# Kernel optimization log

Measured on AMD Instinct MI355X. Metric: run time of the kernel, lower is better.

The kernel has to match this reference:

```python
import jax, jax.numpy as jnp
import numpy as np

NEG_SLOPE = 0.2


def setup_inputs() -> dict:
    key = jax.random.key(0)
    kx, ka, kW, kav = jax.random.split(key, 4)
    B, V, H, D = 8, 2048, 256, 128
    x = jax.random.normal(kx, (B, V, H), dtype=jnp.float32)
    adjacency_matrix = jax.random.randint(ka, (V, V), 0, 2, dtype=jnp.int32)
    W = jax.random.normal(kW, (D, H), dtype=jnp.float32) * 0.05  # Linear(H->D), weight [out,in]
    a = jax.random.normal(kav, (1, 2 * D), dtype=jnp.float32) * 0.05  # Linear(2D->1)
    return {"x": x, "adjacency_matrix": adjacency_matrix, "W": W, "a": a}


def reference(x, adjacency_matrix, W, a):
    B, V, H = x.shape
    D = W.shape[0]
    # p = W(x): [B,V,D]
    p = jnp.einsum('bvh,dh->bvd', x, W)
    # a(cat(p_i, p_j)) == a_left.p_i + a_right.p_j ; leaky_relu applied to the sum (same math,
    # avoids materializing the O(B*V^2*2D) repeat/concat tensor)
    a_left, a_right = a[0, :D], a[0, D:]
    e_i = p @ a_left    # [B,V]
    e_j = p @ a_right   # [B,V]
    scores = jax.nn.leaky_relu(e_i[:, :, None] + e_j[:, None, :], negative_slope=NEG_SLOPE)  # [B,V,V]
    weights = jax.nn.softmax(scores, axis=-1)
    adj = adjacency_matrix.astype(weights.dtype)[None]  # [1,V,V]
    weights_masked = weights * adj
    # renormalize masked weights to the (unmasked) row mass
    weights_masked = weights_masked * (
        jnp.sum(weights, axis=-1, keepdims=True) / jnp.sum(weights_masked, axis=-1, keepdims=True)
    )
    # weighted sum over neighbors j: sum_j w[b,i,j] * p[b,j,:]
    attentioned = jnp.einsum('bij,bjd->bid', weights_masked, p)
    return jax.nn.relu(attentioned)
```

## Files before the change

kernel.cpp:

```cpp
#include <hip/hip_runtime.h>
#include <hip/hip_bf16.h>

#define BATCH 8
#define V 2048
#define H 256
#define D 128

typedef __attribute__((ext_vector_type(8))) _Float16 f16x8;
typedef __attribute__((ext_vector_type(4))) float f32x4;
typedef unsigned int uint32;

static __device__ __forceinline__ uint32 pk2(float lo, float hi) {
  __fp16 __attribute__((ext_vector_type(2))) h = __builtin_amdgcn_cvt_pkrtz(lo, hi);
  uint32 u;
  __builtin_memcpy(&u, &h, 4);
  return u;
}

__global__ __launch_bounds__(256) void k_pack(const int* __restrict__ adj,
                                              const float* __restrict__ W,
                                              const float* __restrict__ a,
                                              unsigned int* __restrict__ pkT,
                                              float* __restrict__ vL,
                                              float* __restrict__ vR,
                                              _Float16* __restrict__ Wh) {
  const int blk = blockIdx.x;
  if (blk < V) {
    const int w = threadIdx.x >> 6, lane = threadIdx.x & 63;
    const int* row = adj + (size_t)blk * V;
#pragma unroll
    for (int it = 0; it < 8; ++it) {
      const int j = it * 256 + w * 64 + lane;
      unsigned long long m = __ballot(row[j] != 0);
      if (lane < 2) {
        const int jw = it * 8 + w * 2 + lane;
        pkT[(size_t)jw * V + blk] = (unsigned int)(m >> (lane * 32));
      }
    }
  } else if (blk == V) {
    const int h = threadIdx.x;
    float sL = 0.f, sR = 0.f;
    for (int d = 0; d < D; ++d) {
      const float wv = W[(size_t)d * H + h];
      sL += wv * a[d];
      sR += wv * a[D + d];
    }
    vL[h] = sL;
    vR[h] = sR;
  } else {
    const int t = threadIdx.x;
    for (int i = 0; i < D; ++i)
      Wh[(size_t)i * H + t] = (_Float16)W[(size_t)i * H + t];
  }
}

__global__ __launch_bounds__(256, 2) void k_proj(const float* __restrict__ x,
                                                 const _Float16* __restrict__ Wh,
                                                 const float* __restrict__ vL,
                                                 const float* __restrict__ vR,
                                                 _Float16* __restrict__ pTf,
                                                 float* __restrict__ ei,
                                                 _Float16* __restrict__ Fh,
                                                 _Float16* __restrict__ Ph) {
  __shared__ char xls[32 * 512];
  __shared__ _Float16 st[128][52];
  const int t = threadIdx.x, lane = t & 63, wave = t >> 6;
  const int b = blockIdx.x >> 6;
  const int jt0 = blockIdx.x & 63;
  const int j0 = jt0 * 32;
  const int kq = lane >> 4, l15 = lane & 15;

  {
    const float4 vl4 = *(const float4*)(vL + lane * 4);
    const float4 vr4 = *(const float4*)(vR + lane * 4);
#pragma unroll
    for (int rr = 0; rr < 8; ++rr) {
      const int row = wave * 8 + rr;
      const float4 xv = *(const float4*)(x + ((size_t)(b * V + j0 + row)) * H + lane * 4);
      uint32 u0 = pk2(xv.x, xv.y), u1 = pk2(xv.z, xv.w);
      const int off = row * 512 + ((lane * 8) ^ ((row & 7) << 4));
      *(uint32*)(xls + off) = u0;
      *(uint32*)(xls + off + 4) = u1;
      float eL = xv.x * vl4.x + xv.y * vl4.y + xv.z * vl4.z + xv.w * vl4.w;
      float eR = xv.x * vr4.x + xv.y * vr4.y + xv.z * vr4.z + xv.w * vr4.w;
#pragma unroll
      for (int off_ = 1; off_ < 64; off_ <<= 1) {
        eL += __shfl_xor(eL, off_, 64);
        eR += __shfl_xor(eR, off_, 64);
      }
      if (lane == 0) {
        const size_t r_ = (size_t)b * V + j0 + row;
        ei[r_] = eL;
        Fh[r_] = (_Float16)__expf(eR);
        Ph[r_] = (_Float16)__expf(0.2f * eR);
      }
    }
  }
  __syncthreads();

  f32x4 acc[2][2];
#pragma unroll
  for (int i_ = 0; i_ < 2; ++i_)
#pragma unroll
    for (int j_ = 0; j_ < 2; ++j_) acc[i_][j_] = (f32x4){0.f, 0.f, 0.f, 0.f};

  const char* wbase = (const char*)Wh + ((size_t)(wave * 32 + l15) * H + kq * 8) * 2;
#pragma unroll
  for (int ks = 0; ks < 8; ++ks) {
    f16x8 aw[2], bx[2];
#pragma unroll
    for (int t_ = 0; t_ < 2; ++t_)
      aw[t_] = *(const f16x8*)(wbase + (t_ * 16 * H + ks * 32) * 2);
#pragma unroll
    for (int jt = 0; jt < 2; ++jt) {
      const int row = jt * 16 + l15;
      bx[jt] = *(const f16x8*)(xls + row * 512 + ((ks * 64 + kq * 16) ^ ((l15 & 7) << 4)));
    }
#pragma unroll
    for (int t_ = 0; t_ < 2; ++t_)
#pragma unroll
      for (int jt = 0; jt < 2; ++jt)
        acc[t_][jt] = __builtin_amdgcn_mfma_f32_16x16x32_f16(aw[t_], bx[jt], acc[t_][jt], 0, 0, 0);
  }

#pragma unroll
  for (int t_ = 0; t_ < 2; ++t_)
#pragma unroll
    for (int jt = 0; jt < 2; ++jt)
#pragma unroll
      for (int r = 0; r < 4; ++r)
        st[(wave * 2 + t_) * 16 + kq * 4 + r][jt * 16 + l15] = (_Float16)acc[t_][jt][r];
  __syncthreads();

  const int c = jt0 >> 1;
  const int ksh = jt0 & 1;
  const int g = t >> 6;
#pragma unroll
  for (int ff = 0; ff < 2; ++ff) {
    const int dt = ff * 4 + g;
    const int dR = dt * 16 + l15;
    const int jc = kq * 8;
    union { unsigned long long ll[2]; f16x8 v; } vv_;
    vv_.ll[0] = *(const unsigned long long*)&st[dR][jc];
    vv_.ll[1] = *(const unsigned long long*)&st[dR][jc + 4];
    *(f16x8*)((char*)pTf +
              (((((size_t)b * 32 + c) * 8 + dt) * 2 + ksh) * 64 + lane) * 16) = vv_.v;
  }
}


typedef union { uint4 v; uint32 u[4]; } U4;
typedef union { uint32 u[4]; f16x8 v; } AFu;
struct PFS {
  U4 FH0, FH1, PH0, PH1;
  uint32 w[2][2];
  AFu AF[2][2];
};

#define PKMUL(d, a, b) asm("v_pk_mul_f16 %0, %1, %2" : "=v"(d) : "v"(a), "v"(b));
#define PKMAX(d, a, b) asm("v_pk_max_f16 %0, %1, %2" : "=v"(d) : "v"(a), "v"(b));

#define WGEN(S)                                                        \
  _Pragma("unroll") for (int ig_ = 0; ig_ < 2; ++ig_) {                \
    const uint32 E2_ = Ei2g[ig_], EP2_ = Eip2g[ig_];                   \
    _Pragma("unroll") for (int ks_ = 0; ks_ < 2; ++ks_) {              \
      const uint32 sh_ = (S).w[ig_][ks_] >> kq8;                       \
      _Pragma("unroll") for (int p_ = 0; p_ < 4; ++p_) {               \
        uint32 t0_, t1_;                                               \
        PKMUL(t0_, E2_, (ks_ ? (S).FH1 : (S).FH0).u[p_])               \
        PKMUL(t1_, EP2_, (ks_ ? (S).PH1 : (S).PH0).u[p_])              \
        PKMAX(t0_, t0_, t1_)                                           \
        const uint32 m_ = ((sh_ << (14 - 2 * p_)) & 0x4000u) |         \
                          ((sh_ << (29 - 2 * p_)) & 0x40000000u);      \
        PKMUL((S).AF[ig_][ks_].u[p_], t0_, m_)                         \
      }                                                                \
    }                                                                  \
  }

#define PFETCH(S, C)                                       \
  {                                                        \
    const char* f_ = fbase + (C) * 128 + kq16;             \
    const char* p_ = pbase + (C) * 128 + kq16;             \
    (S).FH0.v = *(const uint4*)(f_);                       \
    (S).FH1.v = *(const uint4*)(f_ + 64);                  \
    (S).PH0.v = *(const uint4*)(p_);                       \
    (S).PH1.v = *(const uint4*)(p_ + 64);                  \
    (S).w[0][0] = adjpT[(size_t)((C) * 2) * V + iR0];      \
    (S).w[0][1] = adjpT[(size_t)((C) * 2 + 1) * V + iR0];  \
    (S).w[1][0] = adjpT[(size_t)((C) * 2) * V + iR1];      \
    (S).w[1][1] = adjpT[(size_t)((C) * 2 + 1) * V + iR1];  \
  }

#define LOADB(BR, C)                                      \
  {                                                       \
    const char* g_ = gbase + (size_t)(C) * 16384;         \
    _Pragma("unroll") for (int q_ = 0; q_ < 4; ++q_)      \
      BR[q_] = *(const f16x8*)(g_ + q_ * 1024);           \
  }

#define DOMFMA(S, BX)                                                          \
  _Pragma("unroll") for (int ig_ = 0; ig_ < 2; ++ig_)                          \
    _Pragma("unroll") for (int nt_ = 0; nt_ < 2; ++nt_)                        \
      _Pragma("unroll") for (int ks_ = 0; ks_ < 2; ++ks_)                      \
        acc[ig_][nt_][ks_] = __builtin_amdgcn_mfma_f32_16x16x32_f16(           \
            (S).AF[ig_][ks_].v, BX[nt_ * 2 + ks_], acc[ig_][nt_][ks_], 0, 0, 0); \
  _Pragma("unroll") for (int ig_ = 0; ig_ < 2; ++ig_)                          \
    _Pragma("unroll") for (int ks_ = 0; ks_ < 2; ++ks_)                        \
      accS[ig_][ks_] = __builtin_amdgcn_mfma_f32_16x16x32_f16(                 \
          (S).AF[ig_][ks_].v, onesv, accS[ig_][ks_], 0, 0, 0);

#define BODYF(C, SX, BX, SY)   \
  {                            \
    DOMFMA(SX, BX)             \
    WGEN(SY)                   \
    LOADB(BX, (C) + 2)         \
    PFETCH(SX, (C) + 2)        \
  }

__global__ __launch_bounds__(256, 2) void k_attn(
    const _Float16* __restrict__ pTf,
    const float* __restrict__ ei,
    const _Float16* __restrict__ Fht,
    const _Float16* __restrict__ Pht,
    const unsigned int* __restrict__ adjpT,
    float* __restrict__ out) {
  const int t = threadIdx.x, lane = t & 63, wave = t >> 6;
  const int ih = wave >> 1;
  const int dq = wave & 1;
  const int pay = (blockIdx.x & 7) * 64 + (blockIdx.x >> 3);
  const int bdh = pay >> 4;
  const int itl = pay & 15;
  const int b = bdh >> 2, dh = (bdh >> 1) & 1;
  const int it = ((bdh & 1) << 4) | itl;
  const int i0b = it * 64;
  const int kq = lane >> 4;
  const int kq8 = kq * 8;
  const int kq16 = kq * 16;
  const int l15 = lane & 15;
  const int ibase = i0b + ih * 32;
  const int iR0 = ibase + l15;
  const int iR1 = iR0 + 16;

  const float eiv0 = ei[(size_t)b * V + iR0];
  const float eiv1 = ei[(size_t)b * V + iR1];
  uint32 Ei2g[2], Eip2g[2];
  {
    const float e0 = 0.5f * __expf(eiv0), e1 = 0.5f * __expf(eiv1);
    const float p0 = 0.5f * __expf(0.2f * eiv0), p1 = 0.5f * __expf(0.2f * eiv1);
    Ei2g[0] = pk2(e0, e0); Ei2g[1] = pk2(e1, e1);
    Eip2g[0] = pk2(p0, p0); Eip2g[1] = pk2(p1, p1);
  }
  const char* fbase = (const char*)(Fht + (size_t)b * V);
  const char* pbase = (const char*)(Pht + (size_t)b * V);
  const size_t fb0 = ((size_t)b * 32) * 16384 + (size_t)dh * 8192;
  const char* gbase = (const char*)pTf + fb0 + dq * 4096 + lane * 16;

  union { uint32 u[4]; f16x8 v; } ones_;
  ones_.u[0] = ones_.u[1] = ones_.u[2] = ones_.u[3] = 0x3C003C00u;
  const f16x8 onesv = ones_.v;

  f32x4 acc[2][2][2];
#pragma unroll
  for (int a_ = 0; a_ < 2; ++a_)
#pragma unroll
    for (int b_ = 0; b_ < 2; ++b_)
#pragma unroll
      for (int c_ = 0; c_ < 2; ++c_) acc[a_][b_][c_] = (f32x4){0.f, 0.f, 0.f, 0.f};
  f32x4 accS[2][2];
#pragma unroll
  for (int a_ = 0; a_ < 2; ++a_)
#pragma unroll
    for (int c_ = 0; c_ < 2; ++c_) accS[a_][c_] = (f32x4){0.f, 0.f, 0.f, 0.f};

  f16x8 bA[4], bB[4];
  PFS sA, sB;

  LOADB(bA, 0)
  LOADB(bB, 1)
  PFETCH(sA, 0)
  PFETCH(sB, 1)
  WGEN(sA)

  for (int c2 = 0; c2 < 15; ++c2) {
    const int c = c2 * 2;
    BODYF(c, sA, bA, sB)
    BODYF(c + 1, sB, bB, sA)
  }
  {
    DOMFMA(sA, bA)
    WGEN(sB)
  }
  { DOMFMA(sB, bB) }

  float* ob = out + ((size_t)b * V + ibase) * D + dh * 64 + dq * 32 + l15;
#pragma unroll
  for (int ig = 0; ig < 2; ++ig) {
#pragma unroll
    for (int r = 0; r < 4; ++r) {
      const float inv_ = 1.0f / (accS[ig][0][r] + accS[ig][1][r]);
#pragma unroll
      for (int nt = 0; nt < 2; ++nt) {
        const float v = (acc[ig][nt][0][r] + acc[ig][nt][1][r]) * inv_;
        ob[(size_t)(ig * 16 + kq * 4 + r) * D + nt * 16] = fmaxf(v, 0.f);
      }
    }
  }
}

extern "C" void kernel_launch(void* const* d_in, const int* in_sizes, int n_in,
                              void* d_out, int out_size, void* d_ws, size_t ws_size,
                              hipStream_t stream) {
  const float* x = (const float*)d_in[0];
  const int* adj = (const int*)d_in[1];
  const float* W = (const float*)d_in[2];
  const float* a = (const float*)d_in[3];
  float* out = (float*)d_out;

  char* ws = (char*)d_ws;
  _Float16* pTf = (_Float16*)ws;
  float* ei = (float*)(ws + (4u << 20));
  _Float16* Fh = (_Float16*)(ws + (4u << 20) + 65536);
  _Float16* Ph = (_Float16*)(ws + (4u << 20) + 98304);
  unsigned int* adjpT = (unsigned int*)(ws + (4u << 20) + 131072);
  float* vL = (float*)(ws + (4u << 20) + 655360);
  float* vR = (float*)(ws + (4u << 20) + 656384);
  _Float16* Wh = (_Float16*)(ws + (4u << 20) + 657408);

  k_pack<<<dim3(V + 2), dim3(256), 0, stream>>>(adj, W, a, adjpT, vL, vR, Wh);
  k_proj<<<dim3(BATCH * (V / 32)), dim3(256), 0, stream>>>(x, Wh, vL, vR, pTf, ei, Fh, Ph);
  k_attn<<<dim3(BATCH * 2 * (V / 64)), dim3(256), 0, stream>>>(pTf, ei, Fh, Ph, adjpT, out);
}
```

Measured before the change: 54.46 us.

## Split attention over neighbor halves with partial sums and a reduce kernel

The attention kernel now splits the neighbor dimension j into two halves, doubling the grid to 1024 blocks. Each block writes partial weighted sums and row sums to workspace, and a new reduce kernel combines them, normalizes and applies ReLU. The inner loop drops the double-buffered per-stage weight fragments in favour of generating them just before the MFMAs, and launch bounds rise to 4 blocks per CU to lower register pressure and raise occupancy. The cost is extra global traffic for the partials (about 16 MB written and read back), one more launch, and less latency hiding from the shallower software pipeline.

After: 57.01 us. +4.7%, slower.

```diff
diff --git a/kernel.cpp b/kernel.cpp
--- a/kernel.cpp
+++ b/kernel.cpp
@@ -154,13 +154,12 @@
 struct PFS {
   U4 FH0, FH1, PH0, PH1;
   uint32 w[2][2];
-  AFu AF[2][2];
 };
 
 #define PKMUL(d, a, b) asm("v_pk_mul_f16 %0, %1, %2" : "=v"(d) : "v"(a), "v"(b));
 #define PKMAX(d, a, b) asm("v_pk_max_f16 %0, %1, %2" : "=v"(d) : "v"(a), "v"(b));
 
-#define WGEN(S)                                                        \
+#define WGEN(S, AF_)                                                   \
   _Pragma("unroll") for (int ig_ = 0; ig_ < 2; ++ig_) {                \
     const uint32 E2_ = Ei2g[ig_], EP2_ = Eip2g[ig_];                   \
     _Pragma("unroll") for (int ks_ = 0; ks_ < 2; ++ks_) {              \
@@ -172,7 +171,7 @@
         PKMAX(t0_, t0_, t1_)                                           \
         const uint32 m_ = ((sh_ << (14 - 2 * p_)) & 0x4000u) |         \
                           ((sh_ << (29 - 2 * p_)) & 0x40000000u);      \
-        PKMUL((S).AF[ig_][ks_].u[p_], t0_, m_)                         \
+        PKMUL(AF_[ig_][ks_].u[p_], t0_, m_)                            \
       }                                                                \
     }                                                                  \
   }
@@ -185,10 +184,10 @@
     (S).FH1.v = *(const uint4*)(f_ + 64);                  \
     (S).PH0.v = *(const uint4*)(p_);                       \
     (S).PH1.v = *(const uint4*)(p_ + 64);                  \
-    (S).w[0][0] = adjpT[(size_t)((C) * 2) * V + iR0];      \
-    (S).w[0][1] = adjpT[(size_t)((C) * 2 + 1) * V + iR0];  \
-    (S).w[1][0] = adjpT[(size_t)((C) * 2) * V + iR1];      \
-    (S).w[1][1] = adjpT[(size_t)((C) * 2 + 1) * V + iR1];  \
+    (S).w[0][0] = adjb[(size_t)((C) * 2) * V + iR0];       \
+    (S).w[0][1] = adjb[(size_t)((C) * 2 + 1) * V + iR0];   \
+    (S).w[1][0] = adjb[(size_t)((C) * 2) * V + iR1];       \
+    (S).w[1][1] = adjb[(size_t)((C) * 2 + 1) * V + iR1];   \
   }
 
 #define LOADB(BR, C)                                      \
@@ -198,40 +197,44 @@
       BR[q_] = *(const f16x8*)(g_ + q_ * 1024);           \
   }
 
-#define DOMFMA(S, BX)                                                          \
+#define DOMFMA(AF_, BX)                                                        \
   _Pragma("unroll") for (int ig_ = 0; ig_ < 2; ++ig_)                          \
     _Pragma("unroll") for (int nt_ = 0; nt_ < 2; ++nt_)                        \
       _Pragma("unroll") for (int ks_ = 0; ks_ < 2; ++ks_)                      \
         acc[ig_][nt_][ks_] = __builtin_amdgcn_mfma_f32_16x16x32_f16(           \
-            (S).AF[ig_][ks_].v, BX[nt_ * 2 + ks_], acc[ig_][nt_][ks_], 0, 0, 0); \
-  _Pragma("unroll") for (int ig_ = 0; ig_ < 2; ++ig_)                          \
-    _Pragma("unroll") for (int ks_ = 0; ks_ < 2; ++ks_)                        \
-      accS[ig_][ks_] = __builtin_amdgcn_mfma_f32_16x16x32_f16(                 \
-          (S).AF[ig_][ks_].v, onesv, accS[ig_][ks_], 0, 0, 0);
-
-#define BODYF(C, SX, BX, SY)   \
-  {                            \
-    DOMFMA(SX, BX)             \
-    WGEN(SY)                   \
-    LOADB(BX, (C) + 2)         \
-    PFETCH(SX, (C) + 2)        \
-  }
-
-__global__ __launch_bounds__(256, 2) void k_attn(
+            AF_[ig_][ks_].v, BX[nt_ * 2 + ks_], acc[ig_][nt_][ks_], 0, 0, 0);  \
+  _Pragma("unroll") for (int ig_ = 0; ig_ < 2; ++ig_) {                        \
+    accS[ig_] = __builtin_amdgcn_mfma_f32_16x16x32_f16(                        \
+        AF_[ig_][0].v, onesv, accS[ig_], 0, 0, 0);                             \
+    accS[ig_] = __builtin_amdgcn_mfma_f32_16x16x32_f16(                        \
+        AF_[ig_][1].v, onesv, accS[ig_], 0, 0, 0);                             \
+  }
+
+#define BODY(C, BX)                 \
+  {                                 \
+    AFu af_[2][2];                  \
+    WGEN(S, af_)                    \
+    DOMFMA(af_, BX)                 \
+    if ((C) + 2 < 16) LOADB(BX, (C) + 2)  \
+    if ((C) + 1 < 16) PFETCH(S, (C) + 1)  \
+  }
+
+__global__ __launch_bounds__(256, 4) void k_attn(
     const _Float16* __restrict__ pTf,
     const float* __restrict__ ei,
     const _Float16* __restrict__ Fht,
     const _Float16* __restrict__ Pht,
     const unsigned int* __restrict__ adjpT,
-    float* __restrict__ out) {
+    float* __restrict__ pvp,
+    float* __restrict__ rsp) {
   const int t = threadIdx.x, lane = t & 63, wave = t >> 6;
   const int ih = wave >> 1;
   const int dq = wave & 1;
-  const int pay = (blockIdx.x & 7) * 64 + (blockIdx.x >> 3);
-  const int bdh = pay >> 4;
-  const int itl = pay & 15;
-  const int b = bdh >> 2, dh = (bdh >> 1) & 1;
-  const int it = ((bdh & 1) << 4) | itl;
+  const int pay = (blockIdx.x & 7) * 128 + (blockIdx.x >> 3);
+  const int b = pay >> 7;
+  const int dh = (pay >> 6) & 1;
+  const int jh = (pay >> 5) & 1;
+  const int it = pay & 31;
   const int i0b = it * 64;
   const int kq = lane >> 4;
   const int kq8 = kq * 8;
@@ -250,10 +253,12 @@
     Ei2g[0] = pk2(e0, e0); Ei2g[1] = pk2(e1, e1);
     Eip2g[0] = pk2(p0, p0); Eip2g[1] = pk2(p1, p1);
   }
-  const char* fbase = (const char*)(Fht + (size_t)b * V);
-  const char* pbase = (const char*)(Pht + (size_t)b * V);
+  const char* fbase = (const char*)(Fht + (size_t)b * V) + jh * 2048;
+  const char* pbase = (const char*)(Pht + (size_t)b * V) + jh * 2048;
+  const unsigned int* adjb = adjpT + (size_t)(jh * 32) * V;
   const size_t fb0 = ((size_t)b * 32) * 16384 + (size_t)dh * 8192;
-  const char* gbase = (const char*)pTf + fb0 + dq * 4096 + lane * 16;
+  const char* gbase = (const char*)pTf + fb0 + (size_t)jh * 16 * 16384 +
+                      dq * 4096 + lane * 16;
 
   union { uint32 u[4]; f16x8 v; } ones_;
   ones_.u[0] = ones_.u[1] = ones_.u[2] = ones_.u[3] = 0x3C003C00u;
@@ -266,45 +271,59 @@
     for (int b_ = 0; b_ < 2; ++b_)
 #pragma unroll
       for (int c_ = 0; c_ < 2; ++c_) acc[a_][b_][c_] = (f32x4){0.f, 0.f, 0.f, 0.f};
-  f32x4 accS[2][2];
-#pragma unroll
-  for (int a_ = 0; a_ < 2; ++a_)
-#pragma unroll
-    for (int c_ = 0; c_ < 2; ++c_) accS[a_][c_] = (f32x4){0.f, 0.f, 0.f, 0.f};
+  f32x4 accS[2];
+  accS[0] = (f32x4){0.f, 0.f, 0.f, 0.f};
+  accS[1] = (f32x4){0.f, 0.f, 0.f, 0.f};
 
   f16x8 bA[4], bB[4];
-  PFS sA, sB;
+  PFS S;
 
   LOADB(bA, 0)
   LOADB(bB, 1)
-  PFETCH(sA, 0)
-  PFETCH(sB, 1)
-  WGEN(sA)
-
-  for (int c2 = 0; c2 < 15; ++c2) {
-    const int c = c2 * 2;
-    BODYF(c, sA, bA, sB)
-    BODYF(c + 1, sB, bB, sA)
-  }
-  {
-    DOMFMA(sA, bA)
-    WGEN(sB)
-  }
-  { DOMFMA(sB, bB) }
-
-  float* ob = out + ((size_t)b * V + ibase) * D + dh * 64 + dq * 32 + l15;
-#pragma unroll
-  for (int ig = 0; ig < 2; ++ig) {
-#pragma unroll
-    for (int r = 0; r < 4; ++r) {
-      const float inv_ = 1.0f / (accS[ig][0][r] + accS[ig][1][r]);
-#pragma unroll
-      for (int nt = 0; nt < 2; ++nt) {
-        const float v = (acc[ig][nt][0][r] + acc[ig][nt][1][r]) * inv_;
-        ob[(size_t)(ig * 16 + kq * 4 + r) * D + nt * 16] = fmaxf(v, 0.f);
-      }
-    }
-  }
+  PFETCH(S, 0)
+
+  for (int c = 0; c < 16; c += 2) {
+    BODY(c, bA)
+    BODY(c + 1, bB)
+  }
+
+  float* pb = pvp + (size_t)jh * (BATCH * V * D) +
+              ((size_t)b * V + ibase) * D + dh * 64 + dq * 32 + l15;
+#pragma unroll
+  for (int ig = 0; ig < 2; ++ig)
+#pragma unroll
+    for (int r = 0; r < 4; ++r)
+#pragma unroll
+      for (int nt = 0; nt < 2; ++nt)
+        pb[(size_t)(ig * 16 + kq * 4 + r) * D + nt * 16] =
+            acc[ig][nt][0][r] + acc[ig][nt][1][r];
+
+  if (dh == 0 && dq == 0 && l15 == 0) {
+#pragma unroll
+    for (int ig = 0; ig < 2; ++ig)
+#pragma unroll
+      for (int r = 0; r < 4; ++r)
+        rsp[(size_t)jh * (BATCH * V) + (size_t)b * V + ibase + ig * 16 + kq * 4 + r] =
+            accS[ig][r];
+  }
+}
+
+__global__ __launch_bounds__(256) void k_reduce(const float* __restrict__ pvp,
+                                                const float* __restrict__ rsp,
+                                                float* __restrict__ out) {
+  const int gid = blockIdx.x * 256 + threadIdx.x;
+  const int row = gid >> 5;
+  const int c4 = gid & 31;
+  const size_t idx = (size_t)row * D + c4 * 4;
+  const float inv = 1.0f / (rsp[row] + rsp[BATCH * V + row]);
+  const float4 v0 = *(const float4*)(pvp + idx);
+  const float4 v1 = *(const float4*)(pvp + (size_t)(BATCH * V * D) + idx);
+  float4 o;
+  o.x = fmaxf((v0.x + v1.x) * inv, 0.f);
+  o.y = fmaxf((v0.y + v1.y) * inv, 0.f);
+  o.z = fmaxf((v0.z + v1.z) * inv, 0.f);
+  o.w = fmaxf((v0.w + v1.w) * inv, 0.f);
+  *(float4*)(out + idx) = o;
 }
 
 extern "C" void kernel_launch(void* const* d_in, const int* in_sizes, int n_in,
@@ -325,8 +344,11 @@
   float* vL = (float*)(ws + (4u << 20) + 655360);
   float* vR = (float*)(ws + (4u << 20) + 656384);
   _Float16* Wh = (_Float16*)(ws + (4u << 20) + 657408);
+  float* pvp = (float*)(ws + (8u << 20));
+  float* rsp = (float*)(ws + (24u << 20));
 
   k_pack<<<dim3(V + 2), dim3(256), 0, stream>>>(adj, W, a, adjpT, vL, vR, Wh);
   k_proj<<<dim3(BATCH * (V / 32)), dim3(256), 0, stream>>>(x, Wh, vL, vR, pTf, ei, Fh, Ph);
-  k_attn<<<dim3(BATCH * 2 * (V / 64)), dim3(256), 0, stream>>>(pTf, ei, Fh, Ph, adjpT, out);
-}
+  k_attn<<<dim3(BATCH * 2 * 2 * (V / 64)), dim3(256), 0, stream>>>(pTf, ei, Fh, Ph, adjpT, pvp, rsp);
+  k_reduce<<<dim3((BATCH * V * D / 4) / 256), dim3(256), 0, stream>>>(pvp, rsp, out);
+}
```

## Merge adjacency packing and projection into one prep kernel, recompute W vectors per block

Applied to the files above, without the earlier changes.

Fuses the adjacency bit-packing kernel and the projection kernel into a single launch, with separate block ranges for each job. Each projection block now recomputes the W·a vectors into shared memory and converts W to fp16 on the fly from fp32 global loads, instead of reading precomputed vL/vR/Wh buffers. This removes one kernel launch and the serial dependency between the two kernels, at the cost of redundant per-block work (a 128-step reduction over W) and twice the global bytes for W reads.

New measurement: 51.78 us. 1.05x faster.

```diff
diff --git a/kernel.cpp b/kernel.cpp
--- a/kernel.cpp
+++ b/kernel.cpp
@@ -5,6 +5,7 @@
 #define V 2048
 #define H 256
 #define D 128
+#define NPROJ 512
 
 typedef __attribute__((ext_vector_type(8))) _Float16 f16x8;
 typedef __attribute__((ext_vector_type(4))) float f32x4;
@@ -17,62 +18,56 @@
   return u;
 }
 
-__global__ __launch_bounds__(256) void k_pack(const int* __restrict__ adj,
-                                              const float* __restrict__ W,
-                                              const float* __restrict__ a,
-                                              unsigned int* __restrict__ pkT,
-                                              float* __restrict__ vL,
-                                              float* __restrict__ vR,
-                                              _Float16* __restrict__ Wh) {
-  const int blk = blockIdx.x;
-  if (blk < V) {
-    const int w = threadIdx.x >> 6, lane = threadIdx.x & 63;
-    const int* row = adj + (size_t)blk * V;
+__global__ __launch_bounds__(256, 2) void k_prep(const float* __restrict__ x,
+                                                 const int* __restrict__ adj,
+                                                 const float* __restrict__ W,
+                                                 const float* __restrict__ a,
+                                                 _Float16* __restrict__ pTf,
+                                                 float* __restrict__ ei,
+                                                 _Float16* __restrict__ Fh,
+                                                 _Float16* __restrict__ Ph,
+                                                 unsigned int* __restrict__ pkT) {
+  __shared__ char xls[32 * 512];
+  __shared__ _Float16 st[128][52];
+  __shared__ float vls[256], vrs[256];
+  const int t = threadIdx.x, lane = t & 63, wave = t >> 6;
+
+  if (blockIdx.x >= NPROJ) {
+    const int i = blockIdx.x - NPROJ;
+    const int w = wave;
+    const int* row = adj + (size_t)i * V;
 #pragma unroll
     for (int it = 0; it < 8; ++it) {
       const int j = it * 256 + w * 64 + lane;
       unsigned long long m = __ballot(row[j] != 0);
       if (lane < 2) {
         const int jw = it * 8 + w * 2 + lane;
-        pkT[(size_t)jw * V + blk] = (unsigned int)(m >> (lane * 32));
+        pkT[(size_t)jw * V + i] = (unsigned int)(m >> (lane * 32));
       }
     }
-  } else if (blk == V) {
-    const int h = threadIdx.x;
-    float sL = 0.f, sR = 0.f;
-    for (int d = 0; d < D; ++d) {
-      const float wv = W[(size_t)d * H + h];
-      sL += wv * a[d];
-      sR += wv * a[D + d];
-    }
-    vL[h] = sL;
-    vR[h] = sR;
-  } else {
-    const int t = threadIdx.x;
-    for (int i = 0; i < D; ++i)
-      Wh[(size_t)i * H + t] = (_Float16)W[(size_t)i * H + t];
-  }
-}
-
-__global__ __launch_bounds__(256, 2) void k_proj(const float* __restrict__ x,
-                                                 const _Float16* __restrict__ Wh,
-                                                 const float* __restrict__ vL,
-                                                 const float* __restrict__ vR,
-                                                 _Float16* __restrict__ pTf,
-                                                 float* __restrict__ ei,
-                                                 _Float16* __restrict__ Fh,
-                                                 _Float16* __restrict__ Ph) {
-  __shared__ char xls[32 * 512];
-  __shared__ _Float16 st[128][52];
-  const int t = threadIdx.x, lane = t & 63, wave = t >> 6;
+    return;
+  }
+
   const int b = blockIdx.x >> 6;
   const int jt0 = blockIdx.x & 63;
   const int j0 = jt0 * 32;
   const int kq = lane >> 4, l15 = lane & 15;
 
   {
-    const float4 vl4 = *(const float4*)(vL + lane * 4);
-    const float4 vr4 = *(const float4*)(vR + lane * 4);
+    float sL = 0.f, sR = 0.f;
+    for (int d = 0; d < D; ++d) {
+      const float wv = W[(size_t)d * H + t];
+      sL += wv * a[d];
+      sR += wv * a[D + d];
+    }
+    vls[t] = sL;
+    vrs[t] = sR;
+  }
+  __syncthreads();
+
+  {
+    const float4 vl4 = *(const float4*)(vls + lane * 4);
+    const float4 vr4 = *(const float4*)(vrs + lane * 4);
 #pragma unroll
     for (int rr = 0; rr < 8; ++rr) {
       const int row = wave * 8 + rr;
@@ -104,23 +99,29 @@
 #pragma unroll
     for (int j_ = 0; j_ < 2; ++j_) acc[i_][j_] = (f32x4){0.f, 0.f, 0.f, 0.f};
 
-  const char* wbase = (const char*)Wh + ((size_t)(wave * 32 + l15) * H + kq * 8) * 2;
+  typedef union { uint32 u[4]; f16x8 v; } AFu_;
+  const float* wrow0 = W + (size_t)(wave * 32 + l15) * H + kq * 8;
+  const float* wrow1 = wrow0 + 16 * H;
 #pragma unroll
   for (int ks = 0; ks < 8; ++ks) {
-    f16x8 aw[2], bx[2];
-#pragma unroll
-    for (int t_ = 0; t_ < 2; ++t_)
-      aw[t_] = *(const f16x8*)(wbase + (t_ * 16 * H + ks * 32) * 2);
+    const int ho = ks * 32;
+    const float4 w0a = *(const float4*)(wrow0 + ho), w0b = *(const float4*)(wrow0 + ho + 4);
+    const float4 w1a = *(const float4*)(wrow1 + ho), w1b = *(const float4*)(wrow1 + ho + 4);
+    AFu_ aw0, aw1;
+    aw0.u[0] = pk2(w0a.x, w0a.y); aw0.u[1] = pk2(w0a.z, w0a.w);
+    aw0.u[2] = pk2(w0b.x, w0b.y); aw0.u[3] = pk2(w0b.z, w0b.w);
+    aw1.u[0] = pk2(w1a.x, w1a.y); aw1.u[1] = pk2(w1a.z, w1a.w);
+    aw1.u[2] = pk2(w1b.x, w1b.y); aw1.u[3] = pk2(w1b.z, w1b.w);
+    f16x8 bx[2];
 #pragma unroll
     for (int jt = 0; jt < 2; ++jt) {
       const int row = jt * 16 + l15;
       bx[jt] = *(const f16x8*)(xls + row * 512 + ((ks * 64 + kq * 16) ^ ((l15 & 7) << 4)));
     }
-#pragma unroll
-    for (int t_ = 0; t_ < 2; ++t_)
-#pragma unroll
-      for (int jt = 0; jt < 2; ++jt)
-        acc[t_][jt] = __builtin_amdgcn_mfma_f32_16x16x32_f16(aw[t_], bx[jt], acc[t_][jt], 0, 0, 0);
+    acc[0][0] = __builtin_amdgcn_mfma_f32_16x16x32_f16(aw0.v, bx[0], acc[0][0], 0, 0, 0);
+    acc[0][1] = __builtin_amdgcn_mfma_f32_16x16x32_f16(aw0.v, bx[1], acc[0][1], 0, 0, 0);
+    acc[1][0] = __builtin_amdgcn_mfma_f32_16x16x32_f16(aw1.v, bx[0], acc[1][0], 0, 0, 0);
+    acc[1][1] = __builtin_amdgcn_mfma_f32_16x16x32_f16(aw1.v, bx[1], acc[1][1], 0, 0, 0);
   }
 
 #pragma unroll
@@ -147,7 +148,6 @@
               (((((size_t)b * 32 + c) * 8 + dt) * 2 + ksh) * 64 + lane) * 16) = vv_.v;
   }
 }
-
 
 typedef union { uint4 v; uint32 u[4]; } U4;
 typedef union { uint32 u[4]; f16x8 v; } AFu;
@@ -322,11 +322,7 @@
   _Float16* Fh = (_Float16*)(ws + (4u << 20) + 65536);
   _Float16* Ph = (_Float16*)(ws + (4u << 20) + 98304);
   unsigned int* adjpT = (unsigned int*)(ws + (4u << 20) + 131072);
-  float* vL = (float*)(ws + (4u << 20) + 655360);
-  float* vR = (float*)(ws + (4u << 20) + 656384);
-  _Float16* Wh = (_Float16*)(ws + (4u << 20) + 657408);
-
-  k_pack<<<dim3(V + 2), dim3(256), 0, stream>>>(adj, W, a, adjpT, vL, vR, Wh);
-  k_proj<<<dim3(BATCH * (V / 32)), dim3(256), 0, stream>>>(x, Wh, vL, vR, pTf, ei, Fh, Ph);
+
+  k_prep<<<dim3(NPROJ + V), dim3(256), 0, stream>>>(x, adj, W, a, pTf, ei, Fh, Ph, adjpT);
   k_attn<<<dim3(BATCH * 2 * (V / 64)), dim3(256), 0, stream>>>(pTf, ei, Fh, Ph, adjpT, out);
 }
```
